# Kernel tuning notes

Measured on AMD Instinct MI355X. Metric: run time of the kernel, lower is better.

Reference implementation:

```python
import jax, jax.numpy as jnp
import numpy as np

GROUPS = 32
EPS = 1e-5

def setup_inputs() -> dict:
    key = jax.random.key(0)
    k1, k2, k3 = jax.random.split(key, 3)
    C = 512
    x = jax.random.normal(k1, (4, C, 64, 64), dtype=jnp.float32)
    gn_weight = jnp.ones((C,), jnp.float32)
    gn_bias = jnp.zeros((C,), jnp.float32)
    qkv_weight = jax.random.normal(k2, (3 * C, C), jnp.float32) * (1.0 / np.sqrt(C))
    proj_weight = jax.random.normal(k3, (C, C), jnp.float32) * (1.0 / np.sqrt(C))
    proj_bias = jnp.zeros((C,), jnp.float32)
    return {"x": x, "gn_weight": gn_weight, "gn_bias": gn_bias,
            "qkv_weight": qkv_weight, "proj_weight": proj_weight, "proj_bias": proj_bias}

def reference(x, gn_weight, gn_bias, qkv_weight, proj_weight, proj_bias):
    n, c, h, w = x.shape
    residue = x
    # GroupNorm(32, c): normalize over (c//32 channels * h * w) per group
    xg = x.reshape(n, GROUPS, -1)
    mu = xg.mean(axis=-1, keepdims=True)
    var = xg.var(axis=-1, keepdims=True)
    xn = (xg - mu) * jax.lax.rsqrt(var + EPS)
    xn = xn.reshape(n, c, h, w) * gn_weight[None, :, None, None] + gn_bias[None, :, None, None]
    # tokens: [n, T, c] with T = h*w
    t = xn.reshape(n, c, h * w).transpose(0, 2, 1)
    # qkv linear (no bias), n_heads = 1 so head_size = c
    qkv = jnp.einsum('ntc,dc->ntd', t, qkv_weight)
    q, k, v = jnp.split(qkv, 3, axis=-1)
    scale = 1.0 / np.sqrt(c)
    scores = jnp.einsum('nqc,nkc->nqk', q, k) * scale  # [n, T, T]
    weights = jax.nn.softmax(scores, axis=-1)
    out = jnp.einsum('nqk,nkc->nqc', weights, v)
    out = jnp.einsum('ntc,dc->ntd', out, proj_weight) + proj_bias
    out = out.transpose(0, 2, 1).reshape(n, c, h, w)
    return out + residue
```

## Files before the change

### kernel.cpp

```cpp
#include <hip/hip_runtime.h>
#include <hip/hip_bf16.h>

typedef __bf16 bf16;
typedef __bf16 bf16x8 __attribute__((ext_vector_type(8)));
typedef float f32x4 __attribute__((ext_vector_type(4)));

__device__ __forceinline__ void gload_lds16(const bf16* g, bf16* l) {
    __builtin_amdgcn_global_load_lds(
        (const __attribute__((address_space(1))) void*)g,
        (__attribute__((address_space(3))) void*)l, 16, 0, 0);
}

__global__ __launch_bounds__(256) void k_gnstats(const float* __restrict__ x,
                                                 float2* __restrict__ stats) {
    const int g = blockIdx.x;
    const float4* p = (const float4*)(x + (long)g * 65536);
    float s = 0.f, ss = 0.f;
    #pragma unroll 8
    for (int i = 0; i < 64; ++i) {
        float4 v = p[threadIdx.x + i * 256];
        s  += v.x + v.y + v.z + v.w;
        ss += v.x * v.x + v.y * v.y + v.z * v.z + v.w * v.w;
    }
    #pragma unroll
    for (int off = 32; off >= 1; off >>= 1) {
        s  += __shfl_down(s, off);
        ss += __shfl_down(ss, off);
    }
    __shared__ float rs[4], rss[4];
    if ((threadIdx.x & 63) == 0) { rs[threadIdx.x >> 6] = s; rss[threadIdx.x >> 6] = ss; }
    __syncthreads();
    if (threadIdx.x == 0) {
        float S  = rs[0] + rs[1] + rs[2] + rs[3];
        float SS = rss[0] + rss[1] + rss[2] + rss[3];
        float mu = S * (1.f / 65536.f);
        float var = SS * (1.f / 65536.f) - mu * mu;
        stats[g] = make_float2(mu, rsqrtf(var + 1e-5f));
    }
}

__global__ __launch_bounds__(256) void k_norm_t(const float* __restrict__ x,
                                                const float* __restrict__ w,
                                                const float* __restrict__ b,
                                                const float2* __restrict__ stats,
                                                bf16* __restrict__ t) {
    __shared__ float tile[64][65];
    const int bid = blockIdx.x;
    const int n = bid >> 9, rem = bid & 511;
    const int s0 = (rem >> 3) * 64, c0 = (rem & 7) * 64;
    const int tid = threadIdx.x;
    const int sl = tid & 63, cq = tid >> 6;
    #pragma unroll
    for (int i = 0; i < 16; ++i) {
        const int cl = cq * 16 + i;
        const int c = c0 + cl;
        const float2 st = stats[n * 32 + (c >> 4)];
        const float v = x[((long)(n * 512 + c)) * 4096 + s0 + sl];
        tile[cl][sl] = (v - st.x) * st.y * w[c] + b[c];
    }
    __syncthreads();
    #pragma unroll
    for (int i = 0; i < 16; ++i) {
        const int sl2 = cq * 16 + i;
        const int cl2 = tid & 63;
        t[((long)(n * 4096 + s0 + sl2)) * 512 + c0 + cl2] = (bf16)tile[cl2][sl2];
    }
}

__global__ __launch_bounds__(256) void k_convw(const float* __restrict__ qw,
                                               const float* __restrict__ pw,
                                               bf16* __restrict__ qwb,
                                               bf16* __restrict__ pwb) {
    const int i = blockIdx.x * 256 + threadIdx.x;
    if (i < 786432) {
        float v = qw[i];
        if (i < 512 * 512) v *= 0.06376281516217733f;
        qwb[i] = (bf16)v;
    } else {
        const int j = i - 786432;
        pwb[j] = (bf16)pw[j];
    }
}

__global__ __launch_bounds__(256) void k_vt(const bf16* __restrict__ qkv,
                                            bf16* __restrict__ Vt) {
    __shared__ bf16 tile[64][66];
    const int bid = blockIdx.x;
    const int n = bid >> 9, rem = bid & 511;
    const int s0 = (rem >> 3) * 64, d0 = (rem & 7) * 64;
    const int tid = threadIdx.x;
    #pragma unroll
    for (int i = 0; i < 16; ++i) {
        const int sl = (tid >> 6) * 16 + i;
        const int dl = tid & 63;
        tile[sl][dl] = qkv[((long)(n * 4096 + s0 + sl)) * 1536 + 1024 + d0 + dl];
    }
    __syncthreads();
    #pragma unroll
    for (int i = 0; i < 16; ++i) {
        const int dl = (tid >> 6) * 16 + i;
        const int sl = tid & 63;
        Vt[((long)(n * 512 + d0 + dl)) * 4096 + s0 + sl] = tile[sl][dl];
    }
}

#define PH(mh, kk, S_, WN)                                                         \
  {                                                                                \
    if ((mh) == 0) {                                                               \
      _Pragma("unroll")                                                            \
      for (int n = 0; n < 4; ++n) {                                                \
        int row = wn * 64 + n * 16 + lr;                                           \
        int cg = lg ^ (row & 3);                                                   \
        bfr[n] = *(const bf16x8*)(BsT + (kk) * 8192 + row * 32 + cg * 8);          \
      }                                                                            \
    }                                                                              \
    _Pragma("unroll")                                                              \
    for (int i = 0; i < 4; ++i) {                                                  \
      int row = wm * 128 + ((mh) * 4 + i) * 16 + lr;                               \
      int cg = lg ^ (row & 3);                                                     \
      af[i] = *(const bf16x8*)(AsT + (kk) * 8192 + row * 32 + cg * 8);             \
    }                                                                              \
    if ((S_) >= 0) issue_unit(S_);                                                 \
    __builtin_amdgcn_s_barrier();                                                  \
    asm volatile("" ::: "memory");                                                 \
    __builtin_amdgcn_s_setprio(1);                                                 \
    _Pragma("unroll")                                                              \
    for (int i = 0; i < 4; ++i)                                                    \
      _Pragma("unroll")                                                            \
      for (int n = 0; n < 4; ++n)                                                  \
        acc[(mh) * 4 + i][n] =                                                     \
            __builtin_amdgcn_mfma_f32_16x16x32_bf16(af[i], bfr[n],                 \
                                                    acc[(mh) * 4 + i][n], 0, 0, 0);\
    __builtin_amdgcn_s_setprio(0);                                                 \
    if constexpr ((WN) >= 0)                                                       \
      asm volatile("s_waitcnt vmcnt(%0)" ::"i"(WN) : "memory");                    \
    __builtin_amdgcn_s_barrier();                                                  \
    asm volatile("" ::: "memory");                                                 \
  }

template <int EPI>
__global__ __launch_bounds__(512, 2) void gemm256(
    const bf16* __restrict__ A, int lda, long aZ,
    const bf16* __restrict__ B, int ldb, long bZ,
    bf16* __restrict__ C, int ldc, long cZ, int K,
    float* __restrict__ Lp) {
    __shared__ bf16 As[2 * 2 * 256 * 32];
    __shared__ bf16 Bs[2 * 2 * 256 * 32];
    const int t = threadIdx.x;
    const int wid = t >> 6, l = t & 63;
    const int wm = wid >> 2, wn = wid & 3;
    const int lr = l & 15;
    const int lg = l >> 4;
    const long z = blockIdx.z;

    const int gx = gridDim.x;
    int nwg = gx * gridDim.y;
    int flat = blockIdx.y * gx + blockIdx.x;
    if ((nwg & 7) == 0) { int qq = nwg >> 3; flat = (flat & 7) * qq + (flat >> 3); }
    const int bx = flat % gx, by = flat / gx;

    const bf16* Ab = A + z * aZ + (long)bx * 256 * lda;
    const bf16* Bb = B + z * bZ + (long)by * 256 * ldb;

    const int NT = K >> 6;
    const int NT4 = NT << 2;

    f32x4 acc[8][4];
    #pragma unroll
    for (int i = 0; i < 8; ++i)
        #pragma unroll
        for (int n = 0; n < 4; ++n) acc[i][n] = f32x4{0.f, 0.f, 0.f, 0.f};

    const int srow = t >> 2;
    const int scg0 = t & 3;

    auto issue_unit = [&](int s) {
        int ti = s >> 2, idx = s & 3;
        int kh = idx >> 1, isB = idx & 1;
        const bf16* g = isB ? Bb : Ab;
        int ld = isB ? ldb : lda;
        bf16* lp = (isB ? Bs : As) + ((ti & 1) * 2 + kh) * 8192;
        int k0 = ti * 64 + kh * 32;
        #pragma unroll
        for (int j = 0; j < 2; ++j) {
            int row = j * 128 + srow;
            int cg = scg0 ^ (row & 3);
            gload_lds16(g + (long)row * ld + k0 + cg * 8, lp + (j * 512 + t) * 8);
        }
    };

    #pragma unroll
    for (int s = 0; s < 6; ++s) issue_unit(s);
    asm volatile("s_waitcnt vmcnt(8)" ::: "memory");
    __builtin_amdgcn_s_barrier();
    asm volatile("" ::: "memory");

    bf16x8 bfr[4], af[4];

    for (int ti = 0; ti < NT - 2; ++ti) {
        const bf16* AsT = As + (ti & 1) * 16384;
        const bf16* BsT = Bs + (ti & 1) * 16384;
        const int sb = 4 * ti + 6;
        PH(0, 0, sb + 0, -1)
        PH(1, 0, sb + 1, 8)
        PH(0, 1, sb + 2, -1)
        PH(1, 1, sb + 3, 8)
    }
    {
        const bf16* AsT = As + ((NT - 2) & 1) * 16384;
        const bf16* BsT = Bs + ((NT - 2) & 1) * 16384;
        PH(0, 0, NT4 - 2, -1)
        PH(1, 0, NT4 - 1, 8)
        PH(0, 1, -1, -1)
        PH(1, 1, -1, 4)
    }
    {
        const bf16* AsT = As + ((NT - 1) & 1) * 16384;
        const bf16* BsT = Bs + ((NT - 1) & 1) * 16384;
        PH(0, 0, -1, -1)
        PH(1, 0, -1, 0)
        PH(0, 1, -1, -1)
        PH(1, 1, -1, -1)
    }

    const int row0 = bx * 256 + wm * 128;
    const int col0 = by * 256 + wn * 64;
    const int rq = lg * 4;
    bf16* Cz = C + z * cZ;

    if (EPI == 1) {
        float rs[8][4];
        #pragma unroll
        for (int i = 0; i < 8; ++i)
            #pragma unroll
            for (int r = 0; r < 4; ++r) rs[i][r] = 0.f;
        #pragma unroll
        for (int i = 0; i < 8; ++i)
            #pragma unroll
            for (int n = 0; n < 4; ++n) {
                const int col = col0 + n * 16 + lr;
                #pragma unroll
                for (int r = 0; r < 4; ++r) {
                    float p = exp2f(acc[i][n][r]);
                    rs[i][r] += p;
                    Cz[(long)(row0 + i * 16 + rq + r) * ldc + col] = (bf16)p;
                }
            }
        #pragma unroll
        for (int i = 0; i < 8; ++i)
            #pragma unroll
            for (int r = 0; r < 4; ++r) {
                float s = rs[i][r];
                s += __shfl_xor(s, 1);
                s += __shfl_xor(s, 2);
                s += __shfl_xor(s, 4);
                s += __shfl_xor(s, 8);
                rs[i][r] = s;
            }
        float* lsf = (float*)As;
        if (lr == 0) {
            #pragma unroll
            for (int i = 0; i < 8; ++i)
                #pragma unroll
                for (int r = 0; r < 4; ++r)
                    lsf[wn * 256 + wm * 128 + i * 16 + lg * 4 + r] = rs[i][r];
        }
        __syncthreads();
        if (t < 256) {
            float v = lsf[t] + lsf[256 + t] + lsf[512 + t] + lsf[768 + t];
            Lp[((long)z * 16 + by) * 4096 + bx * 256 + t] = v;
        }
    } else {
        #pragma unroll
        for (int i = 0; i < 8; ++i)
            #pragma unroll
            for (int n = 0; n < 4; ++n) {
                const int col = col0 + n * 16 + lr;
                #pragma unroll
                for (int r = 0; r < 4; ++r)
                    Cz[(long)(row0 + i * 16 + rq + r) * ldc + col] = (bf16)acc[i][n][r];
            }
    }
}

__global__ __launch_bounds__(512, 1) void k_pv(
    const bf16* __restrict__ P, const float* __restrict__ Lp,
    const bf16* __restrict__ Vt, bf16* __restrict__ O) {
    __shared__ bf16 Bs[2][512 * 64];
    __shared__ bf16 As[2][64 * 64];
    __shared__ float linv[64];
    const int t = threadIdx.x;
    const int w = t >> 6, l = t & 63, lr = l & 15, lg = l >> 4;
    const int lr7 = lr & 7;
    const int sr = t >> 3, sc8 = t & 7, sr7 = sr & 7;
    const long z = blockIdx.y;
    const int bx = blockIdx.x;

    const bf16* Pg = P + z * ((long)4096 * 4096) + (long)(bx * 64 + sr) * 4096 + (sc8 ^ sr7) * 8;
    const bf16* Vg = Vt + z * ((long)512 * 4096) + (long)sr * 4096 + (sc8 ^ sr7) * 8;

    auto issue = [&](int tile, int buf) {
        gload_lds16(Pg + tile * 64, As[buf] + t * 8);
        #pragma unroll
        for (int u = 0; u < 8; ++u)
            gload_lds16(Vg + (long)u * 64 * 4096 + tile * 64, Bs[buf] + u * 4096 + t * 8);
    };

    if (t < 64) {
        const float* lpp = Lp + z * 16 * 4096 + bx * 64 + t;
        float s = 0.f;
        #pragma unroll
        for (int j = 0; j < 16; ++j) s += lpp[j * 4096];
        linv[t] = 1.f / s;
    }

    f32x4 acc[4][4];
    #pragma unroll
    for (int i = 0; i < 4; ++i)
        #pragma unroll
        for (int n = 0; n < 4; ++n) acc[i][n] = f32x4{0.f, 0.f, 0.f, 0.f};

    issue(0, 0);
    issue(1, 1);

    for (int ti = 0; ti < 64; ++ti) {
        if (ti < 63) { asm volatile("s_waitcnt vmcnt(9)" ::: "memory"); }
        else         { asm volatile("s_waitcnt vmcnt(0)" ::: "memory"); }
        __builtin_amdgcn_s_barrier();
        asm volatile("" ::: "memory");

        const bf16* Asb = As[ti & 1];
        const bf16* Bsb = Bs[ti & 1];
        __builtin_amdgcn_s_setprio(1);
        #pragma unroll
        for (int kk = 0; kk < 2; ++kk) {
            bf16x8 af[4], bfv[4];
            #pragma unroll
            for (int mi = 0; mi < 4; ++mi)
                af[mi] = *(const bf16x8*)(Asb + (mi * 16 + lr) * 64 + (((kk * 4 + lg) ^ lr7) * 8));
            #pragma unroll
            for (int n = 0; n < 4; ++n)
                bfv[n] = *(const bf16x8*)(Bsb + (w * 64 + n * 16 + lr) * 64 + (((kk * 4 + lg) ^ lr7) * 8));
            #pragma unroll
            for (int mi = 0; mi < 4; ++mi)
                #pragma unroll
                for (int n = 0; n < 4; ++n)
                    acc[mi][n] = __builtin_amdgcn_mfma_f32_16x16x32_bf16(af[mi], bfv[n], acc[mi][n], 0, 0, 0);
        }
        __builtin_amdgcn_s_setprio(0);

        __builtin_amdgcn_s_barrier();
        asm volatile("" ::: "memory");
        if (ti < 62) issue(ti + 2, ti & 1);
    }

    bf16* Oz = O + z * ((long)4096 * 512);
    #pragma unroll
    for (int mi = 0; mi < 4; ++mi) {
        float4 lv = *(const float4*)&linv[mi * 16 + lg * 4];
        #pragma unroll
        for (int n = 0; n < 4; ++n) {
            const long base = (long)(bx * 64 + mi * 16 + lg * 4) * 512 + w * 64 + n * 16 + lr;
            Oz[base]        = (bf16)(acc[mi][n][0] * lv.x);
            Oz[base + 512]  = (bf16)(acc[mi][n][1] * lv.y);
            Oz[base + 1024] = (bf16)(acc[mi][n][2] * lv.z);
            Oz[base + 1536] = (bf16)(acc[mi][n][3] * lv.w);
        }
    }
}

#define PH128(nh, kk, S_, WN)                                                      \
  {                                                                                \
    if ((nh) == 0) {                                                               \
      _Pragma("unroll")                                                            \
      for (int i = 0; i < 4; ++i) {                                                \
        int row = wm * 64 + i * 16 + lr;                                           \
        int cg = lg ^ (row & 3);                                                   \
        af[i] = *(const bf16x8*)(AsT + (kk) * 8192 + row * 32 + cg * 8);           \
      }                                                                            \
    }                                                                              \
    _Pragma("unroll")                                                              \
    for (int j = 0; j < 2; ++j) {                                                  \
      int row = wn * 64 + ((nh) * 2 + j) * 16 + lr;                                \
      int cg = lg ^ (row & 3);                                                     \
      bfr[j] = *(const bf16x8*)(BsT + (kk) * 4096 + row * 32 + cg * 8);            \
    }                                                                              \
    if ((S_) >= 0) issue_unit(S_);                                                 \
    __builtin_amdgcn_s_barrier();                                                  \
    asm volatile("" ::: "memory");                                                 \
    __builtin_amdgcn_s_setprio(1);                                                 \
    _Pragma("unroll")                                                              \
    for (int i = 0; i < 4; ++i)                                                    \
      _Pragma("unroll")                                                            \
      for (int j = 0; j < 2; ++j)                                                  \
        acc[i][(nh) * 2 + j] =                                                     \
            __builtin_amdgcn_mfma_f32_16x16x32_bf16(af[i], bfr[j],                 \
                                                    acc[i][(nh) * 2 + j], 0, 0, 0);\
    __builtin_amdgcn_s_setprio(0);                                                 \
    if constexpr ((WN) >= 0)                                                       \
      asm volatile("s_waitcnt vmcnt(%0)" ::"i"(WN) : "memory");                    \
    __builtin_amdgcn_s_barrier();                                                  \
    asm volatile("" ::: "memory");                                                 \
  }

template <int EPI>
__global__ __launch_bounds__(512, 2) void gemm_n128(
    const bf16* __restrict__ A, int lda, long aZ,
    const bf16* __restrict__ B, int ldb, long bZ,
    void* __restrict__ Cvp, int ldc, long cZ, int K,
    const float* __restrict__ bias) {
    __shared__ bf16 As[2 * 2 * 256 * 32];
    __shared__ bf16 Bs[2 * 2 * 128 * 32];
    const int t = threadIdx.x;
    const int wid = t >> 6, l = t & 63;
    const int wm = wid >> 1, wn = wid & 1;
    const int lr = l & 15;
    const int lg = l >> 4;
    const long z = blockIdx.z;

    const int gx = gridDim.x;
    int nwg = gx * gridDim.y;
    int flat = blockIdx.y * gx + blockIdx.x;
    if ((nwg & 7) == 0) { int qq = nwg >> 3; flat = (flat & 7) * qq + (flat >> 3); }
    const int bx = flat % gx, by = flat / gx;

    const bf16* Ab = A + z * aZ + (long)bx * 256 * lda;
    const bf16* Bb = B + z * bZ + (long)by * 128 * ldb;

    const int NT = K >> 6;
    const int NT4 = NT << 2;

    f32x4 acc[4][4];
    #pragma unroll
    for (int i = 0; i < 4; ++i)
        #pragma unroll
        for (int n = 0; n < 4; ++n) acc[i][n] = f32x4{0.f, 0.f, 0.f, 0.f};

    const int srow = t >> 2;
    const int scg0 = t & 3;

    auto issue_unit = [&](int s) {
        int ti = s >> 2, idx = s & 3;
        int kh = idx >> 1, isB = idx & 1;
        int k0 = ti * 64 + kh * 32;
        if (isB) {
            bf16* lp = Bs + ((ti & 1) * 2 + kh) * 4096;
            int cg = scg0 ^ (srow & 3);
            gload_lds16(Bb + (long)srow * ldb + k0 + cg * 8, lp + t * 8);
        } else {
            bf16* lp = As + ((ti & 1) * 2 + kh) * 8192;
            #pragma unroll
            for (int j = 0; j < 2; ++j) {
                int row = j * 128 + srow;
                int cg = scg0 ^ (row & 3);
                gload_lds16(Ab + (long)row * lda + k0 + cg * 8, lp + (j * 512 + t) * 8);
            }
        }
    };

    #pragma unroll
    for (int s = 0; s < 6; ++s) issue_unit(s);
    asm volatile("s_waitcnt vmcnt(6)" ::: "memory");
    __builtin_amdgcn_s_barrier();
    asm volatile("" ::: "memory");

    bf16x8 bfr[2], af[4];

    for (int ti = 0; ti < NT - 2; ++ti) {
        const bf16* AsT = As + (ti & 1) * 16384;
        const bf16* BsT = Bs + (ti & 1) * 8192;
        const int sb = 4 * ti + 6;
        PH128(0, 0, sb + 0, -1)
        PH128(1, 0, sb + 1, 6)
        PH128(0, 1, sb + 2, -1)
        PH128(1, 1, sb + 3, 6)
    }
    {
        const bf16* AsT = As + ((NT - 2) & 1) * 16384;
        const bf16* BsT = Bs + ((NT - 2) & 1) * 8192;
        PH128(0, 0, NT4 - 2, -1)
        PH128(1, 0, NT4 - 1, 6)
        PH128(0, 1, -1, -1)
        PH128(1, 1, -1, 3)
    }
    {
        const bf16* AsT = As + ((NT - 1) & 1) * 16384;
        const bf16* BsT = Bs + ((NT - 1) & 1) * 8192;
        PH128(0, 0, -1, -1)
        PH128(1, 0, -1, 0)
        PH128(0, 1, -1, -1)
        PH128(1, 1, -1, -1)
    }

    const int row0 = bx * 256 + wm * 64;
    const int col0 = by * 128 + wn * 64;
    const int rq = lg * 4;
    if (EPI == 2) {
        float* C = (float*)Cvp + z * cZ;
        #pragma unroll
        for (int i = 0; i < 4; ++i)
            #pragma unroll
            for (int n = 0; n < 4; ++n) {
                const int col = col0 + n * 16 + lr;
                #pragma unroll
                for (int r = 0; r < 4; ++r)
                    C[(long)(row0 + i * 16 + rq + r) * ldc + col] = acc[i][n][r] + bias[col];
            }
    } else {
        bf16* C = (bf16*)Cvp + z * cZ;
        #pragma unroll
        for (int i = 0; i < 4; ++i)
            #pragma unroll
            for (int n = 0; n < 4; ++n) {
                const int col = col0 + n * 16 + lr;
                #pragma unroll
                for (int r = 0; r < 4; ++r)
                    C[(long)(row0 + i * 16 + rq + r) * ldc + col] = (bf16)acc[i][n][r];
            }
    }
}

__global__ __launch_bounds__(256) void k_final(const float* __restrict__ pb,
                                               const float* __restrict__ x,
                                               float* __restrict__ out) {
    __shared__ float tile[64][65];
    const int bid = blockIdx.x;
    const int n = bid >> 9, rem = bid & 511;
    const int s0 = (rem >> 3) * 64, c0 = (rem & 7) * 64;
    const int tid = threadIdx.x;
    #pragma unroll
    for (int i = 0; i < 16; ++i) {
        const int sl = (tid >> 6) * 16 + i;
        const int cl = tid & 63;
        tile[sl][cl] = pb[((long)(n * 4096 + s0 + sl)) * 512 + c0 + cl];
    }
    __syncthreads();
    #pragma unroll
    for (int i = 0; i < 16; ++i) {
        const int cl = (tid >> 6) * 16 + i;
        const int sl = tid & 63;
        const long oi = ((long)(n * 512 + c0 + cl)) * 4096 + s0 + sl;
        out[oi] = tile[sl][cl] + x[oi];
    }
}

extern "C" void kernel_launch(void* const* d_in, const int* in_sizes, int n_in,
                              void* d_out, int out_size, void* d_ws, size_t ws_size,
                              hipStream_t stream) {
    const float* x     = (const float*)d_in[0];
    const float* gnw   = (const float*)d_in[1];
    const float* gnb   = (const float*)d_in[2];
    const float* qkvw  = (const float*)d_in[3];
    const float* projw = (const float*)d_in[4];
    const float* projb = (const float*)d_in[5];

    char* ws = (char*)d_ws;
    size_t off = 0;
    auto alloc = [&](size_t bytes) {
        void* p = ws + off;
        off += (bytes + 255) & ~(size_t)255;
        return p;
    };
    bf16*   qwb   = (bf16*)alloc((size_t)1536 * 512 * 2);
    bf16*   pwb   = (bf16*)alloc((size_t)512 * 512 * 2);
    float2* stats = (float2*)alloc((size_t)128 * 8);
    bf16*   tbuf  = (bf16*)alloc((size_t)16384 * 512 * 2);
    bf16*   qkv   = (bf16*)alloc((size_t)16384 * 1536 * 2);
    bf16*   Vt    = (bf16*)alloc((size_t)4 * 512 * 4096 * 2);
    float*  Lpart = (float*)alloc((size_t)4 * 16 * 4096 * 4);
    const size_t SSZ = (size_t)4096 * 4096 * 2;
    const size_t fixed = off;
    int g = 1;
    if (ws_size >= fixed + 4 * SSZ) g = 4;
    else if (ws_size >= fixed + 2 * SSZ) g = 2;
    bf16* Sbuf = (bf16*)alloc(g * SSZ);

    k_gnstats<<<128, 256, 0, stream>>>(x, stats);
    k_norm_t<<<2048, 256, 0, stream>>>(x, gnw, gnb, stats, tbuf);
    k_convw<<<4096, 256, 0, stream>>>(qkvw, projw, qwb, pwb);

    gemm256<0><<<dim3(64, 6, 1), 512, 0, stream>>>(
        tbuf, 512, 0, qwb, 512, 0, qkv, 1536, 0, 512, nullptr);

    k_vt<<<2048, 256, 0, stream>>>(qkv, Vt);

    const long TS = (long)4096 * 1536;
    for (int g0 = 0; g0 < 4; g0 += g) {
        gemm256<1><<<dim3(16, 16, g), 512, 0, stream>>>(
            qkv + (long)g0 * TS, 1536, TS,
            qkv + (long)g0 * TS + 512, 1536, TS,
            Sbuf, 4096, (long)4096 * 4096, 512, Lpart);
        k_pv<<<dim3(64, g), 512, 0, stream>>>(
            Sbuf, Lpart, Vt + (long)g0 * 512 * 4096, tbuf + (long)g0 * 4096 * 512);
    }

    gemm_n128<2><<<dim3(64, 4, 1), 512, 0, stream>>>(
        tbuf, 512, 0, pwb, 512, 0, (float*)Sbuf, 512, 0, 512, projb);

    k_final<<<2048, 256, 0, stream>>>((float*)Sbuf, x, (float*)d_out);
}
```

Before: 312.5 us.

## Make GEMM persistent over multiple output tiles and move softmax exp into PV kernel

```diff
diff --git a/kernel.cpp b/kernel.cpp
--- a/kernel.cpp
+++ b/kernel.cpp
@@ -138,12 +138,11 @@
     asm volatile("" ::: "memory");                                                 \
   }
 
-template <int EPI>
-__global__ __launch_bounds__(512, 2) void gemm256(
-    const bf16* __restrict__ A, int lda, long aZ,
-    const bf16* __restrict__ B, int ldb, long bZ,
-    bf16* __restrict__ C, int ldc, long cZ, int K,
-    float* __restrict__ Lp) {
+template <int NTILES>
+__global__ __launch_bounds__(512, 2) void gemm256p(
+    const bf16* __restrict__ A, int lda, long dA,
+    const bf16* __restrict__ B, int ldb, long dB,
+    bf16* __restrict__ C, int ldc, long dC) {
     __shared__ bf16 As[2 * 2 * 256 * 32];
     __shared__ bf16 Bs[2 * 2 * 256 * 32];
     const int t = threadIdx.x;
@@ -151,7 +150,6 @@
     const int wm = wid >> 2, wn = wid & 3;
     const int lr = l & 15;
     const int lg = l >> 4;
-    const long z = blockIdx.z;
 
     const int gx = gridDim.x;
     int nwg = gx * gridDim.y;
@@ -159,11 +157,10 @@
     if ((nwg & 7) == 0) { int qq = nwg >> 3; flat = (flat & 7) * qq + (flat >> 3); }
     const int bx = flat % gx, by = flat / gx;
 
-    const bf16* Ab = A + z * aZ + (long)bx * 256 * lda;
-    const bf16* Bb = B + z * bZ + (long)by * 256 * ldb;
-
-    const int NT = K >> 6;
-    const int NT4 = NT << 2;
+    const long bxoff = (long)bx * 256 * lda;
+    const long byoff = (long)by * 256 * ldb;
+
+    constexpr int GT = NTILES * 8;
 
     f32x4 acc[8][4];
     #pragma unroll
@@ -175,102 +172,26 @@
     const int scg0 = t & 3;
 
     auto issue_unit = [&](int s) {
-        int ti = s >> 2, idx = s & 3;
+        int tig = s >> 2, idx = s & 3;
+        int j = tig >> 3, til = tig & 7;
         int kh = idx >> 1, isB = idx & 1;
-        const bf16* g = isB ? Bb : Ab;
+        const bf16* g = isB ? (B + (long)j * dB + byoff) : (A + (long)j * dA + bxoff);
         int ld = isB ? ldb : lda;
-        bf16* lp = (isB ? Bs : As) + ((ti & 1) * 2 + kh) * 8192;
-        int k0 = ti * 64 + kh * 32;
-        #pragma unroll
-        for (int j = 0; j < 2; ++j) {
-            int row = j * 128 + srow;
+        bf16* lp = (isB ? Bs : As) + ((tig & 1) * 2 + kh) * 8192;
+        int k0 = til * 64 + kh * 32;
+        #pragma unroll
+        for (int jj = 0; jj < 2; ++jj) {
+            int row = jj * 128 + srow;
             int cg = scg0 ^ (row & 3);
-            gload_lds16(g + (long)row * ld + k0 + cg * 8, lp + (j * 512 + t) * 8);
+            gload_lds16(g + (long)row * ld + k0 + cg * 8, lp + (jj * 512 + t) * 8);
         }
     };
 
-    #pragma unroll
-    for (int s = 0; s < 6; ++s) issue_unit(s);
-    asm volatile("s_waitcnt vmcnt(8)" ::: "memory");
-    __builtin_amdgcn_s_barrier();
-    asm volatile("" ::: "memory");
-
-    bf16x8 bfr[4], af[4];
-
-    for (int ti = 0; ti < NT - 2; ++ti) {
-        const bf16* AsT = As + (ti & 1) * 16384;
-        const bf16* BsT = Bs + (ti & 1) * 16384;
-        const int sb = 4 * ti + 6;
-        PH(0, 0, sb + 0, -1)
-        PH(1, 0, sb + 1, 8)
-        PH(0, 1, sb + 2, -1)
-        PH(1, 1, sb + 3, 8)
-    }
-    {
-        const bf16* AsT = As + ((NT - 2) & 1) * 16384;
-        const bf16* BsT = Bs + ((NT - 2) & 1) * 16384;
-        PH(0, 0, NT4 - 2, -1)
-        PH(1, 0, NT4 - 1, 8)
-        PH(0, 1, -1, -1)
-        PH(1, 1, -1, 4)
-    }
-    {
-        const bf16* AsT = As + ((NT - 1) & 1) * 16384;
-        const bf16* BsT = Bs + ((NT - 1) & 1) * 16384;
-        PH(0, 0, -1, -1)
-        PH(1, 0, -1, 0)
-        PH(0, 1, -1, -1)
-        PH(1, 1, -1, -1)
-    }
-
-    const int row0 = bx * 256 + wm * 128;
-    const int col0 = by * 256 + wn * 64;
-    const int rq = lg * 4;
-    bf16* Cz = C + z * cZ;
-
-    if (EPI == 1) {
-        float rs[8][4];
-        #pragma unroll
-        for (int i = 0; i < 8; ++i)
-            #pragma unroll
-            for (int r = 0; r < 4; ++r) rs[i][r] = 0.f;
-        #pragma unroll
-        for (int i = 0; i < 8; ++i)
-            #pragma unroll
-            for (int n = 0; n < 4; ++n) {
-                const int col = col0 + n * 16 + lr;
-                #pragma unroll
-                for (int r = 0; r < 4; ++r) {
-                    float p = exp2f(acc[i][n][r]);
-                    rs[i][r] += p;
-                    Cz[(long)(row0 + i * 16 + rq + r) * ldc + col] = (bf16)p;
-                }
-            }
-        #pragma unroll
-        for (int i = 0; i < 8; ++i)
-            #pragma unroll
-            for (int r = 0; r < 4; ++r) {
-                float s = rs[i][r];
-                s += __shfl_xor(s, 1);
-                s += __shfl_xor(s, 2);
-                s += __shfl_xor(s, 4);
-                s += __shfl_xor(s, 8);
-                rs[i][r] = s;
-            }
-        float* lsf = (float*)As;
-        if (lr == 0) {
-            #pragma unroll
-            for (int i = 0; i < 8; ++i)
-                #pragma unroll
-                for (int r = 0; r < 4; ++r)
-                    lsf[wn * 256 + wm * 128 + i * 16 + lg * 4 + r] = rs[i][r];
-        }
-        __syncthreads();
-        if (t < 256) {
-            float v = lsf[t] + lsf[256 + t] + lsf[512 + t] + lsf[768 + t];
-            Lp[((long)z * 16 + by) * 4096 + bx * 256 + t] = v;
-        }
-    } else {
+    auto store_tile = [&](int j) {
+        bf16* Cz = C + (long)j * dC;
+        const int row0 = bx * 256 + wm * 128;
+        const int col0 = by * 256 + wn * 64;
+        const int rq = lg * 4;
         #pragma unroll
         for (int i = 0; i < 8; ++i)
             #pragma unroll
@@ -280,12 +201,53 @@
                 for (int r = 0; r < 4; ++r)
                     Cz[(long)(row0 + i * 16 + rq + r) * ldc + col] = (bf16)acc[i][n][r];
             }
-    }
+        #pragma unroll
+        for (int i = 0; i < 8; ++i)
+            #pragma unroll
+            for (int n = 0; n < 4; ++n) acc[i][n] = f32x4{0.f, 0.f, 0.f, 0.f};
+    };
+
+    #pragma unroll
+    for (int s = 0; s < 6; ++s) issue_unit(s);
+    asm volatile("s_waitcnt vmcnt(8)" ::: "memory");
+    __builtin_amdgcn_s_barrier();
+    asm volatile("" ::: "memory");
+
+    bf16x8 bfr[4], af[4];
+
+    #pragma unroll 1
+    for (int gt = 0; gt < GT - 2; ++gt) {
+        const bf16* AsT = As + (gt & 1) * 16384;
+        const bf16* BsT = Bs + (gt & 1) * 16384;
+        const int sb = 4 * gt + 6;
+        PH(0, 0, sb + 0, -1)
+        PH(1, 0, sb + 1, 8)
+        PH(0, 1, sb + 2, -1)
+        PH(1, 1, sb + 3, 8)
+        if (NTILES > 1 && (gt & 7) == 7) store_tile(gt >> 3);
+    }
+    {
+        const bf16* AsT = As + ((GT - 2) & 1) * 16384;
+        const bf16* BsT = Bs + ((GT - 2) & 1) * 16384;
+        PH(0, 0, 4 * GT - 2, -1)
+        PH(1, 0, 4 * GT - 1, 8)
+        PH(0, 1, -1, -1)
+        PH(1, 1, -1, 4)
+    }
+    {
+        const bf16* AsT = As + ((GT - 1) & 1) * 16384;
+        const bf16* BsT = Bs + ((GT - 1) & 1) * 16384;
+        PH(0, 0, -1, -1)
+        PH(1, 0, -1, 0)
+        PH(0, 1, -1, -1)
+        PH(1, 1, -1, -1)
+    }
+    store_tile(NTILES - 1);
 }
 
 __global__ __launch_bounds__(512, 1) void k_pv(
-    const bf16* __restrict__ P, const float* __restrict__ Lp,
-    const bf16* __restrict__ Vt, bf16* __restrict__ O) {
+    const bf16* __restrict__ S, const bf16* __restrict__ Vt,
+    bf16* __restrict__ O) {
     __shared__ bf16 Bs[2][512 * 64];
     __shared__ bf16 As[2][64 * 64];
     __shared__ float linv[64];
@@ -296,23 +258,31 @@
     const long z = blockIdx.y;
     const int bx = blockIdx.x;
 
-    const bf16* Pg = P + z * ((long)4096 * 4096) + (long)(bx * 64 + sr) * 4096 + (sc8 ^ sr7) * 8;
+    const bf16* Sg = S + z * ((long)4096 * 4096) + (long)(bx * 64 + sr) * 4096 + (sc8 ^ sr7) * 8;
     const bf16* Vg = Vt + z * ((long)512 * 4096) + (long)sr * 4096 + (sc8 ^ sr7) * 8;
 
     auto issue = [&](int tile, int buf) {
-        gload_lds16(Pg + tile * 64, As[buf] + t * 8);
+        gload_lds16(Sg + tile * 64, As[buf] + t * 8);
         #pragma unroll
         for (int u = 0; u < 8; ++u)
             gload_lds16(Vg + (long)u * 64 * 4096 + tile * 64, Bs[buf] + u * 4096 + t * 8);
     };
 
-    if (t < 64) {
-        const float* lpp = Lp + z * 16 * 4096 + bx * 64 + t;
+    float lsum = 0.f;
+    auto exppass = [&](int buf) {
+        bf16* slot = As[buf] + t * 8;
+        bf16x8 sv = *(bf16x8*)slot;
+        bf16x8 pv;
         float s = 0.f;
         #pragma unroll
-        for (int j = 0; j < 16; ++j) s += lpp[j * 4096];
-        linv[t] = 1.f / s;
-    }
+        for (int j = 0; j < 8; ++j) {
+            float e = exp2f((float)sv[j]);
+            s += e;
+            pv[j] = (bf16)e;
+        }
+        *(bf16x8*)slot = pv;
+        lsum += s;
+    };
 
     f32x4 acc[4][4];
     #pragma unroll
@@ -322,10 +292,10 @@
 
     issue(0, 0);
     issue(1, 1);
+    asm volatile("s_waitcnt vmcnt(9)" ::: "memory");
+    exppass(0);
 
     for (int ti = 0; ti < 64; ++ti) {
-        if (ti < 63) { asm volatile("s_waitcnt vmcnt(9)" ::: "memory"); }
-        else         { asm volatile("s_waitcnt vmcnt(0)" ::: "memory"); }
         __builtin_amdgcn_s_barrier();
         asm volatile("" ::: "memory");
 
@@ -352,7 +322,20 @@
         __builtin_amdgcn_s_barrier();
         asm volatile("" ::: "memory");
         if (ti < 62) issue(ti + 2, ti & 1);
-    }
+        if (ti < 63) {
+            if (ti < 62) { asm volatile("s_waitcnt vmcnt(9)" ::: "memory"); }
+            else         { asm volatile("s_waitcnt vmcnt(0)" ::: "memory"); }
+            exppass((ti + 1) & 1);
+        }
+    }
+
+    lsum += __shfl_xor(lsum, 1);
+    lsum += __shfl_xor(lsum, 2);
+    lsum += __shfl_xor(lsum, 4);
+    if (sc8 == 0) linv[sr] = 1.f / lsum;
+    asm volatile("s_waitcnt lgkmcnt(0)" ::: "memory");
+    __builtin_amdgcn_s_barrier();
+    asm volatile("" ::: "memory");
 
     bf16* Oz = O + z * ((long)4096 * 512);
     #pragma unroll
@@ -567,7 +550,6 @@
     bf16*   tbuf  = (bf16*)alloc((size_t)16384 * 512 * 2);
     bf16*   qkv   = (bf16*)alloc((size_t)16384 * 1536 * 2);
     bf16*   Vt    = (bf16*)alloc((size_t)4 * 512 * 4096 * 2);
-    float*  Lpart = (float*)alloc((size_t)4 * 16 * 4096 * 4);
     const size_t SSZ = (size_t)4096 * 4096 * 2;
     const size_t fixed = off;
     int g = 1;
@@ -579,19 +561,24 @@
     k_norm_t<<<2048, 256, 0, stream>>>(x, gnw, gnb, stats, tbuf);
     k_convw<<<4096, 256, 0, stream>>>(qkvw, projw, qwb, pwb);
 
-    gemm256<0><<<dim3(64, 6, 1), 512, 0, stream>>>(
-        tbuf, 512, 0, qwb, 512, 0, qkv, 1536, 0, 512, nullptr);
+    gemm256p<2><<<dim3(64, 3), 512, 0, stream>>>(
+        tbuf, 512, 0, qwb, 512, (long)768 * 512, qkv, 1536, 768);
 
     k_vt<<<2048, 256, 0, stream>>>(qkv, Vt);
 
     const long TS = (long)4096 * 1536;
+    const long SZ = (long)4096 * 4096;
     for (int g0 = 0; g0 < 4; g0 += g) {
-        gemm256<1><<<dim3(16, 16, g), 512, 0, stream>>>(
-            qkv + (long)g0 * TS, 1536, TS,
-            qkv + (long)g0 * TS + 512, 1536, TS,
-            Sbuf, 4096, (long)4096 * 4096, 512, Lpart);
+        const bf16* qb = qkv + (long)g0 * TS;
+        const bf16* kb = qkv + (long)g0 * TS + 512;
+        if (g == 4)
+            gemm256p<4><<<dim3(16, 16), 512, 0, stream>>>(qb, 1536, TS, kb, 1536, TS, Sbuf, 4096, SZ);
+        else if (g == 2)
+            gemm256p<2><<<dim3(16, 16), 512, 0, stream>>>(qb, 1536, TS, kb, 1536, TS, Sbuf, 4096, SZ);
+        else
+            gemm256p<1><<<dim3(16, 16), 512, 0, stream>>>(qb, 1536, TS, kb, 1536, TS, Sbuf, 4096, SZ);
         k_pv<<<dim3(64, g), 512, 0, stream>>>(
-            Sbuf, Lpart, Vt + (long)g0 * 512 * 4096, tbuf + (long)g0 * 4096 * 512);
+            Sbuf, Vt + (long)g0 * 512 * 4096, tbuf + (long)g0 * 4096 * 512);
     }
 
     gemm_n128<2><<<dim3(64, 4, 1), 512, 0, stream>>>(
```

Result: slower. 325.7 us (+4.2%).

## Fuse V transpose, softmax row sums and residual add into GEMM epilogues

Applied to the files above, without the earlier changes.

```diff
diff --git a/kernel.cpp b/kernel.cpp
--- a/kernel.cpp
+++ b/kernel.cpp
@@ -2,6 +2,7 @@
 #include <hip/hip_bf16.h>
 
 typedef __bf16 bf16;
+typedef __bf16 bf16x4 __attribute__((ext_vector_type(4)));
 typedef __bf16 bf16x8 __attribute__((ext_vector_type(8)));
 typedef float f32x4 __attribute__((ext_vector_type(4)));
 
@@ -79,28 +80,6 @@
     } else {
         const int j = i - 786432;
         pwb[j] = (bf16)pw[j];
-    }
-}
-
-__global__ __launch_bounds__(256) void k_vt(const bf16* __restrict__ qkv,
-                                            bf16* __restrict__ Vt) {
-    __shared__ bf16 tile[64][66];
-    const int bid = blockIdx.x;
-    const int n = bid >> 9, rem = bid & 511;
-    const int s0 = (rem >> 3) * 64, d0 = (rem & 7) * 64;
-    const int tid = threadIdx.x;
-    #pragma unroll
-    for (int i = 0; i < 16; ++i) {
-        const int sl = (tid >> 6) * 16 + i;
-        const int dl = tid & 63;
-        tile[sl][dl] = qkv[((long)(n * 4096 + s0 + sl)) * 1536 + 1024 + d0 + dl];
-    }
-    __syncthreads();
-    #pragma unroll
-    for (int i = 0; i < 16; ++i) {
-        const int dl = (tid >> 6) * 16 + i;
-        const int sl = tid & 63;
-        Vt[((long)(n * 512 + d0 + dl)) * 4096 + s0 + sl] = tile[sl][dl];
     }
 }
 
@@ -140,10 +119,10 @@
 
 template <int EPI>
 __global__ __launch_bounds__(512, 2) void gemm256(
-    const bf16* __restrict__ A, int lda, long aZ,
-    const bf16* __restrict__ B, int ldb, long bZ,
-    bf16* __restrict__ C, int ldc, long cZ, int K,
-    float* __restrict__ Lp) {
+    const bf16* __restrict__ A, int lda,
+    const bf16* __restrict__ B, int ldb,
+    bf16* __restrict__ C, int ldc, int K,
+    bf16* __restrict__ Vt) {
     __shared__ bf16 As[2 * 2 * 256 * 32];
     __shared__ bf16 Bs[2 * 2 * 256 * 32];
     const int t = threadIdx.x;
@@ -151,7 +130,6 @@
     const int wm = wid >> 2, wn = wid & 3;
     const int lr = l & 15;
     const int lg = l >> 4;
-    const long z = blockIdx.z;
 
     const int gx = gridDim.x;
     int nwg = gx * gridDim.y;
@@ -159,8 +137,8 @@
     if ((nwg & 7) == 0) { int qq = nwg >> 3; flat = (flat & 7) * qq + (flat >> 3); }
     const int bx = flat % gx, by = flat / gx;
 
-    const bf16* Ab = A + z * aZ + (long)bx * 256 * lda;
-    const bf16* Bb = B + z * bZ + (long)by * 256 * ldb;
+    const bf16* Ab = A + (long)bx * 256 * lda;
+    const bf16* Bb = B + (long)by * 256 * ldb;
 
     const int NT = K >> 6;
     const int NT4 = NT << 2;
@@ -226,51 +204,8 @@
     const int row0 = bx * 256 + wm * 128;
     const int col0 = by * 256 + wn * 64;
     const int rq = lg * 4;
-    bf16* Cz = C + z * cZ;
 
     if (EPI == 1) {
-        float rs[8][4];
-        #pragma unroll
-        for (int i = 0; i < 8; ++i)
-            #pragma unroll
-            for (int r = 0; r < 4; ++r) rs[i][r] = 0.f;
-        #pragma unroll
-        for (int i = 0; i < 8; ++i)
-            #pragma unroll
-            for (int n = 0; n < 4; ++n) {
-                const int col = col0 + n * 16 + lr;
-                #pragma unroll
-                for (int r = 0; r < 4; ++r) {
-                    float p = exp2f(acc[i][n][r]);
-                    rs[i][r] += p;
-                    Cz[(long)(row0 + i * 16 + rq + r) * ldc + col] = (bf16)p;
-                }
-            }
-        #pragma unroll
-        for (int i = 0; i < 8; ++i)
-            #pragma unroll
-            for (int r = 0; r < 4; ++r) {
-                float s = rs[i][r];
-                s += __shfl_xor(s, 1);
-                s += __shfl_xor(s, 2);
-                s += __shfl_xor(s, 4);
-                s += __shfl_xor(s, 8);
-                rs[i][r] = s;
-            }
-        float* lsf = (float*)As;
-        if (lr == 0) {
-            #pragma unroll
-            for (int i = 0; i < 8; ++i)
-                #pragma unroll
-                for (int r = 0; r < 4; ++r)
-                    lsf[wn * 256 + wm * 128 + i * 16 + lg * 4 + r] = rs[i][r];
-        }
-        __syncthreads();
-        if (t < 256) {
-            float v = lsf[t] + lsf[256 + t] + lsf[512 + t] + lsf[768 + t];
-            Lp[((long)z * 16 + by) * 4096 + bx * 256 + t] = v;
-        }
-    } else {
         #pragma unroll
         for (int i = 0; i < 8; ++i)
             #pragma unroll
@@ -278,14 +213,35 @@
                 const int col = col0 + n * 16 + lr;
                 #pragma unroll
                 for (int r = 0; r < 4; ++r)
-                    Cz[(long)(row0 + i * 16 + rq + r) * ldc + col] = (bf16)acc[i][n][r];
+                    C[(long)(row0 + i * 16 + rq + r) * ldc + col] = (bf16)exp2f(acc[i][n][r]);
             }
+    } else {
+        #pragma unroll
+        for (int i = 0; i < 8; ++i) {
+            const int row = row0 + i * 16 + rq;
+            #pragma unroll
+            for (int n = 0; n < 4; ++n) {
+                const int col = col0 + n * 16 + lr;
+                if (col < 1024) {
+                    #pragma unroll
+                    for (int r = 0; r < 4; ++r)
+                        C[(long)(row + r) * ldc + col] = (bf16)acc[i][n][r];
+                } else {
+                    const int nb = row >> 12;
+                    const int sp = row & 4095;
+                    bf16x4 tmp;
+                    #pragma unroll
+                    for (int r = 0; r < 4; ++r) tmp[r] = (bf16)acc[i][n][r];
+                    *(bf16x4*)(Vt + ((long)nb * 512 + (col - 1024)) * 4096 + sp) = tmp;
+                }
+            }
+        }
     }
 }
 
 __global__ __launch_bounds__(512, 1) void k_pv(
-    const bf16* __restrict__ P, const float* __restrict__ Lp,
-    const bf16* __restrict__ Vt, bf16* __restrict__ O) {
+    const bf16* __restrict__ P, const bf16* __restrict__ Vt,
+    bf16* __restrict__ O) {
     __shared__ bf16 Bs[2][512 * 64];
     __shared__ bf16 As[2][64 * 64];
     __shared__ float linv[64];
@@ -306,19 +262,13 @@
             gload_lds16(Vg + (long)u * 64 * 4096 + tile * 64, Bs[buf] + u * 4096 + t * 8);
     };
 
-    if (t < 64) {
-        const float* lpp = Lp + z * 16 * 4096 + bx * 64 + t;
-        float s = 0.f;
-        #pragma unroll
-        for (int j = 0; j < 16; ++j) s += lpp[j * 4096];
-        linv[t] = 1.f / s;
-    }
-
     f32x4 acc[4][4];
     #pragma unroll
     for (int i = 0; i < 4; ++i)
         #pragma unroll
         for (int n = 0; n < 4; ++n) acc[i][n] = f32x4{0.f, 0.f, 0.f, 0.f};
+
+    float lsum = 0.f;
 
     issue(0, 0);
     issue(1, 1);
@@ -331,6 +281,13 @@
 
         const bf16* Asb = As[ti & 1];
         const bf16* Bsb = Bs[ti & 1];
+
+        {
+            bf16x8 sv = *(const bf16x8*)(Asb + t * 8);
+            #pragma unroll
+            for (int j = 0; j < 8; ++j) lsum += (float)sv[j];
+        }
+
         __builtin_amdgcn_s_setprio(1);
         #pragma unroll
         for (int kk = 0; kk < 2; ++kk) {
@@ -353,6 +310,14 @@
         asm volatile("" ::: "memory");
         if (ti < 62) issue(ti + 2, ti & 1);
     }
+
+    lsum += __shfl_xor(lsum, 1);
+    lsum += __shfl_xor(lsum, 2);
+    lsum += __shfl_xor(lsum, 4);
+    if (sc8 == 0) linv[sr] = 1.f / lsum;
+    asm volatile("s_waitcnt lgkmcnt(0)" ::: "memory");
+    __builtin_amdgcn_s_barrier();
+    asm volatile("" ::: "memory");
 
     bf16* Oz = O + z * ((long)4096 * 512);
     #pragma unroll
@@ -403,12 +368,12 @@
     asm volatile("" ::: "memory");                                                 \
   }
 
-template <int EPI>
-__global__ __launch_bounds__(512, 2) void gemm_n128(
-    const bf16* __restrict__ A, int lda, long aZ,
-    const bf16* __restrict__ B, int ldb, long bZ,
-    void* __restrict__ Cvp, int ldc, long cZ, int K,
-    const float* __restrict__ bias) {
+__global__ __launch_bounds__(512, 2) void gemm_proj(
+    const bf16* __restrict__ A, int lda,
+    const bf16* __restrict__ B, int ldb,
+    const float* __restrict__ bias,
+    const float* __restrict__ xres,
+    float* __restrict__ out) {
     __shared__ bf16 As[2 * 2 * 256 * 32];
     __shared__ bf16 Bs[2 * 2 * 128 * 32];
     const int t = threadIdx.x;
@@ -416,7 +381,6 @@
     const int wm = wid >> 1, wn = wid & 1;
     const int lr = l & 15;
     const int lg = l >> 4;
-    const long z = blockIdx.z;
 
     const int gx = gridDim.x;
     int nwg = gx * gridDim.y;
@@ -424,11 +388,11 @@
     if ((nwg & 7) == 0) { int qq = nwg >> 3; flat = (flat & 7) * qq + (flat >> 3); }
     const int bx = flat % gx, by = flat / gx;
 
-    const bf16* Ab = A + z * aZ + (long)bx * 256 * lda;
-    const bf16* Bb = B + z * bZ + (long)by * 128 * ldb;
-
-    const int NT = K >> 6;
-    const int NT4 = NT << 2;
+    const bf16* Ab = A + (long)bx * 256 * lda;
+    const bf16* Bb = B + (long)by * 128 * ldb;
+
+    const int NT = 8;
+    const int NT4 = 32;
 
     f32x4 acc[4][4];
     #pragma unroll
@@ -495,52 +459,24 @@
     const int row0 = bx * 256 + wm * 64;
     const int col0 = by * 128 + wn * 64;
     const int rq = lg * 4;
-    if (EPI == 2) {
-        float* C = (float*)Cvp + z * cZ;
-        #pragma unroll
-        for (int i = 0; i < 4; ++i)
-            #pragma unroll
-            for (int n = 0; n < 4; ++n) {
-                const int col = col0 + n * 16 + lr;
-                #pragma unroll
-                for (int r = 0; r < 4; ++r)
-                    C[(long)(row0 + i * 16 + rq + r) * ldc + col] = acc[i][n][r] + bias[col];
-            }
-    } else {
-        bf16* C = (bf16*)Cvp + z * cZ;
-        #pragma unroll
-        for (int i = 0; i < 4; ++i)
-            #pragma unroll
-            for (int n = 0; n < 4; ++n) {
-                const int col = col0 + n * 16 + lr;
-                #pragma unroll
-                for (int r = 0; r < 4; ++r)
-                    C[(long)(row0 + i * 16 + rq + r) * ldc + col] = (bf16)acc[i][n][r];
-            }
-    }
-}
-
-__global__ __launch_bounds__(256) void k_final(const float* __restrict__ pb,
-                                               const float* __restrict__ x,
-                                               float* __restrict__ out) {
-    __shared__ float tile[64][65];
-    const int bid = blockIdx.x;
-    const int n = bid >> 9, rem = bid & 511;
-    const int s0 = (rem >> 3) * 64, c0 = (rem & 7) * 64;
-    const int tid = threadIdx.x;
-    #pragma unroll
-    for (int i = 0; i < 16; ++i) {
-        const int sl = (tid >> 6) * 16 + i;
-        const int cl = tid & 63;
-        tile[sl][cl] = pb[((long)(n * 4096 + s0 + sl)) * 512 + c0 + cl];
-    }
-    __syncthreads();
-    #pragma unroll
-    for (int i = 0; i < 16; ++i) {
-        const int cl = (tid >> 6) * 16 + i;
-        const int sl = tid & 63;
-        const long oi = ((long)(n * 512 + c0 + cl)) * 4096 + s0 + sl;
-        out[oi] = tile[sl][cl] + x[oi];
+    #pragma unroll
+    for (int i = 0; i < 4; ++i) {
+        const int row = row0 + i * 16 + rq;
+        const int nb = row >> 12;
+        const int sp = row & 4095;
+        #pragma unroll
+        for (int n = 0; n < 4; ++n) {
+            const int col = col0 + n * 16 + lr;
+            const long off = ((long)nb * 512 + col) * 4096 + sp;
+            const float bb = bias[col];
+            float4 xv = *(const float4*)(xres + off);
+            float4 ov;
+            ov.x = acc[i][n][0] + bb + xv.x;
+            ov.y = acc[i][n][1] + bb + xv.y;
+            ov.z = acc[i][n][2] + bb + xv.z;
+            ov.w = acc[i][n][3] + bb + xv.w;
+            *(float4*)(out + off) = ov;
+        }
     }
 }
 
@@ -567,35 +503,25 @@
     bf16*   tbuf  = (bf16*)alloc((size_t)16384 * 512 * 2);
     bf16*   qkv   = (bf16*)alloc((size_t)16384 * 1536 * 2);
     bf16*   Vt    = (bf16*)alloc((size_t)4 * 512 * 4096 * 2);
-    float*  Lpart = (float*)alloc((size_t)4 * 16 * 4096 * 4);
-    const size_t SSZ = (size_t)4096 * 4096 * 2;
-    const size_t fixed = off;
-    int g = 1;
-    if (ws_size >= fixed + 4 * SSZ) g = 4;
-    else if (ws_size >= fixed + 2 * SSZ) g = 2;
-    bf16* Sbuf = (bf16*)alloc(g * SSZ);
+    bf16*   Sbuf  = (bf16*)alloc((size_t)4096 * 4096 * 2);
 
     k_gnstats<<<128, 256, 0, stream>>>(x, stats);
     k_norm_t<<<2048, 256, 0, stream>>>(x, gnw, gnb, stats, tbuf);
     k_convw<<<4096, 256, 0, stream>>>(qkvw, projw, qwb, pwb);
 
-    gemm256<0><<<dim3(64, 6, 1), 512, 0, stream>>>(
-        tbuf, 512, 0, qwb, 512, 0, qkv, 1536, 0, 512, nullptr);
-
-    k_vt<<<2048, 256, 0, stream>>>(qkv, Vt);
+    gemm256<2><<<dim3(64, 6), 512, 0, stream>>>(
+        tbuf, 512, qwb, 512, qkv, 1536, 512, Vt);
 
     const long TS = (long)4096 * 1536;
-    for (int g0 = 0; g0 < 4; g0 += g) {
-        gemm256<1><<<dim3(16, 16, g), 512, 0, stream>>>(
-            qkv + (long)g0 * TS, 1536, TS,
-            qkv + (long)g0 * TS + 512, 1536, TS,
-            Sbuf, 4096, (long)4096 * 4096, 512, Lpart);
-        k_pv<<<dim3(64, g), 512, 0, stream>>>(
-            Sbuf, Lpart, Vt + (long)g0 * 512 * 4096, tbuf + (long)g0 * 4096 * 512);
-    }
-
-    gemm_n128<2><<<dim3(64, 4, 1), 512, 0, stream>>>(
-        tbuf, 512, 0, pwb, 512, 0, (float*)Sbuf, 512, 0, 512, projb);
-
-    k_final<<<2048, 256, 0, stream>>>((float*)Sbuf, x, (float*)d_out);
-}
+    for (int g0 = 0; g0 < 4; ++g0) {
+        gemm256<1><<<dim3(16, 16), 512, 0, stream>>>(
+            qkv + (long)g0 * TS, 1536,
+            qkv + (long)g0 * TS + 512, 1536,
+            Sbuf, 4096, 512, nullptr);
+        k_pv<<<dim3(64, 1), 512, 0, stream>>>(
+            Sbuf, Vt + (long)g0 * 512 * 4096, tbuf + (long)g0 * 4096 * 512);
+    }
+
+    gemm_proj<<<dim3(64, 4), 512, 0, stream>>>(
+        tbuf, 512, pwb, 512, projb, x, (float*)d_out);
+}
```

Result: slower. 572.1 us (+83.1%).
